# Optimization experiments

Hardware: AMD Instinct MI355X
Metric: run time of the kernel (lower is better)

The kernel has to match this reference:

```python
import jax, jax.numpy as jnp
import numpy as np

B, SENSORY, STATE, MOTOR = 4096, 64, 128, 32
ODE_UNFOLDS = 6
EPS = 1e-8
ELAPSED_TIME = 1.0


def setup_inputs() -> dict:
    key = jax.random.key(0)
    ks = jax.random.split(key, 20)
    u = lambda k, shape, lo, hi: jax.random.uniform(k, shape, jnp.float32, lo, hi)
    sign = lambda k, shape: jnp.where(jax.random.bernoulli(k, 0.5, shape), 1.0, -1.0).astype(jnp.float32)
    mask = lambda k, shape: (jax.random.uniform(k, shape) < 0.75).astype(jnp.float32)
    return {
        "inputs": jax.random.normal(ks[0], (B, SENSORY), jnp.float32),
        "states": jax.random.normal(ks[1], (B, STATE), jnp.float32),
        "gleak": u(ks[2], (STATE,), 0.001, 1.0),
        "vleak": u(ks[3], (STATE,), -0.2, 0.2),
        "cm": u(ks[4], (STATE,), 0.4, 0.6),
        "w": u(ks[5], (STATE, STATE), 0.001, 1.0),
        "sigma": u(ks[6], (STATE, STATE), 3.0, 8.0),
        "mu": u(ks[7], (STATE, STATE), 0.3, 0.8),
        "erev": sign(ks[8], (STATE, STATE)),
        "sensory_w": u(ks[9], (SENSORY, STATE), 0.001, 1.0),
        "sensory_sigma": u(ks[10], (SENSORY, STATE), 3.0, 8.0),
        "sensory_mu": u(ks[11], (SENSORY, STATE), 0.3, 0.8),
        "sensory_erev": sign(ks[12], (SENSORY, STATE)),
        "sparsity_mask": mask(ks[13], (STATE, STATE)),
        "sensory_sparsity_mask": mask(ks[14], (SENSORY, STATE)),
        "input_w": jnp.ones((SENSORY,), jnp.float32),
        "input_b": jnp.zeros((SENSORY,), jnp.float32),
        "output_w": jnp.ones((MOTOR,), jnp.float32),
        "output_b": jnp.zeros((MOTOR,), jnp.float32),
    }


def _syn_sigmoid(v_pre, mu, sigma):
    # v_pre: [B, P] -> [B, P, 1]; mu/sigma: [P, S]
    return jax.nn.sigmoid(sigma * (v_pre[..., None] - mu))


def reference(inputs, states, gleak, vleak, cm, w, sigma, mu, erev,
              sensory_w, sensory_sigma, sensory_mu, sensory_erev,
              sparsity_mask, sensory_sparsity_mask,
              input_w, input_b, output_w, output_b):
    # input mapping (affine); make_positive_fn = Identity (explicit constraints)
    x = inputs * input_w + input_b

    # sensory contributions (computed once, shared across unfolds)
    sens_act = sensory_w * _syn_sigmoid(x, sensory_mu, sensory_sigma)  # [B, In, S]
    sens_act = sens_act * sensory_sparsity_mask
    w_num_sensory = jnp.sum(sens_act * sensory_erev, axis=1)  # [B, S]
    w_den_sensory = jnp.sum(sens_act, axis=1)                 # [B, S]

    cm_t = cm / (ELAPSED_TIME / ODE_UNFOLDS)  # [S]

    v_pre = states
    for _ in range(ODE_UNFOLDS):
        w_act = w * _syn_sigmoid(v_pre, mu, sigma)   # [B, S, S]
        w_act = w_act * sparsity_mask
        w_numerator = jnp.sum(w_act * erev, axis=1) + w_num_sensory
        w_denominator = jnp.sum(w_act, axis=1) + w_den_sensory
        numerator = cm_t * v_pre + gleak * vleak + w_numerator
        denominator = cm_t + gleak + w_denominator
        v_pre = numerator / (denominator + EPS)

    # output mapping: slice motor neurons, then affine
    output = v_pre[:, :MOTOR] * output_w + output_b
    return output, v_pre
```

## Files before the change

kernel.cpp:

```cpp
#include <hip/hip_runtime.h>

#define LOG2E 1.4426950408889634f

constexpr int Bsz = 4096, Ssz = 128, Isz = 64, MOTOR = 32;
constexpr int BT = 4, NT = 256, R = 2;

__global__ void ltc_prep(const float* __restrict__ w, const float* __restrict__ sigma,
                         const float* __restrict__ mu, const float* __restrict__ erev,
                         const float* __restrict__ smask,
                         const float* __restrict__ sw, const float* __restrict__ ssig,
                         const float* __restrict__ smu, const float* __restrict__ serev,
                         const float* __restrict__ ssmask,
                         float4* __restrict__ Tm, float4* __restrict__ Ts)
{
  int idx = blockIdx.x * blockDim.x + threadIdx.x;
  if (idx < 32 * Ssz) {
    int q = idx >> 7, s = idx & 127;
    float4 a, b, wv;
    #pragma unroll
    for (int jj = 0; jj < 4; ++jj) {
      int e = (q * 4 + jj) * Ssz + s;
      float sg = sigma[e];
      (&a.x)[jj] = -sg * LOG2E;
      (&b.x)[jj] = sg * mu[e] * LOG2E;
      (&wv.x)[jj] = w[e] * smask[e] * erev[e];
    }
    Tm[(q * 3 + 0) * Ssz + s] = a;
    Tm[(q * 3 + 1) * Ssz + s] = b;
    Tm[(q * 3 + 2) * Ssz + s] = wv;
  } else if (idx < 32 * Ssz + 16 * Ssz) {
    int k = idx - 32 * Ssz;
    int q = k >> 7, s = k & 127;
    float4 a, b, wv;
    #pragma unroll
    for (int jj = 0; jj < 4; ++jj) {
      int e = (q * 4 + jj) * Ssz + s;
      float sg = ssig[e];
      (&a.x)[jj] = -sg * LOG2E;
      (&b.x)[jj] = sg * smu[e] * LOG2E;
      (&wv.x)[jj] = sw[e] * ssmask[e] * serev[e];
    }
    Ts[(q * 3 + 0) * Ssz + s] = a;
    Ts[(q * 3 + 1) * Ssz + s] = b;
    Ts[(q * 3 + 2) * Ssz + s] = wv;
  }
}

__launch_bounds__(NT, 4)
__global__ void ltc_main(const float* __restrict__ inputs, const float* __restrict__ states,
                         const float* __restrict__ gleak, const float* __restrict__ vleak,
                         const float* __restrict__ cmv,
                         const float* __restrict__ iw, const float* __restrict__ ib,
                         const float* __restrict__ ow, const float* __restrict__ ob,
                         const float4* __restrict__ Tm, const float4* __restrict__ Ts,
                         float* __restrict__ out)
{
  __shared__ float vsh[2][BT][Ssz];
  __shared__ float xsh[BT][Isz];

  const int t = threadIdx.x;
  const int s = t & 127;
  const int r0 = (t >> 7) * R;
  const int b0 = blockIdx.x * BT;

  { int r = t >> 6, i = t & 63;
    xsh[r][i] = inputs[(b0 + r) * Isz + i] * iw[i] + ib[i]; }
  for (int k = t; k < BT * Ssz; k += NT) {
    int r = k >> 7, ss = k & 127;
    vsh[0][r][ss] = states[(b0 + r) * Ssz + ss];
  }
  const float cmt = cmv[s] * 6.0f;
  const float gl = gleak[s];
  const float gv = gl * vleak[s];
  const float dbase = cmt + gl + 1e-8f;
  __syncthreads();

  float sn[R] = {0.f, 0.f}, sd[R] = {0.f, 0.f};
  {
    const float4* pb = Ts + 1 * Ssz + s;
    #pragma unroll 2
    for (int q = 0; q < 16; ++q) {
      float4 a4 = pb[-Ssz], b4 = pb[0], w4 = pb[Ssz];
      pb += 3 * Ssz;
      #pragma unroll
      for (int r = 0; r < R; ++r) {
        float4 xq = *(const float4*)&xsh[r0 + r][q * 4];
        #pragma unroll
        for (int jj = 0; jj < 4; ++jj) {
          float arg = fmaf((&a4.x)[jj], (&xq.x)[jj], (&b4.x)[jj]);
          float u = __builtin_amdgcn_exp2f(arg);
          float sig = __builtin_amdgcn_rcpf(1.0f + u);
          sn[r] = fmaf((&w4.x)[jj], sig, sn[r]);
          sd[r] = fmaf(fabsf((&w4.x)[jj]), sig, sd[r]);
        }
      }
    }
  }

  #pragma unroll 1
  for (int it = 0; it < 6; ++it) {
    const int cur = it & 1;
    const float* vcur = &vsh[cur][0][0];
    float num[R], den[R];
    #pragma unroll
    for (int r = 0; r < R; ++r) { num[r] = sn[r]; den[r] = sd[r]; }

    const float4* pb = Tm + 1 * Ssz + s;
    #pragma unroll 2
    for (int q = 0; q < 32; ++q) {
      float4 a4 = pb[-Ssz], b4 = pb[0], w4 = pb[Ssz];
      pb += 3 * Ssz;
      #pragma unroll
      for (int r = 0; r < R; ++r) {
        float4 vq = *(const float4*)&vcur[(r0 + r) * Ssz + q * 4];
        #pragma unroll
        for (int jj = 0; jj < 4; ++jj) {
          float arg = fmaf((&a4.x)[jj], (&vq.x)[jj], (&b4.x)[jj]);
          float u = __builtin_amdgcn_exp2f(arg);
          float sig = __builtin_amdgcn_rcpf(1.0f + u);
          num[r] = fmaf((&w4.x)[jj], sig, num[r]);
          den[r] = fmaf(fabsf((&w4.x)[jj]), sig, den[r]);
        }
      }
    }

    #pragma unroll
    for (int r = 0; r < R; ++r) {
      float vo = vcur[(r0 + r) * Ssz + s];
      vsh[cur ^ 1][r0 + r][s] =
          (fmaf(cmt, vo, gv) + num[r]) * __builtin_amdgcn_rcpf(dbase + den[r]);
    }
    __syncthreads();
  }

  for (int k = t; k < BT * Ssz; k += NT) {
    int r = k >> 7, ss = k & 127;
    out[Bsz * MOTOR + (b0 + r) * Ssz + ss] = vsh[0][r][ss];
  }
  if (t < BT * MOTOR) {
    int r = t >> 5, m = t & 31;
    out[(b0 + r) * MOTOR + m] = fmaf(vsh[0][r][m], ow[m], ob[m]);
  }
}

extern "C" void kernel_launch(void* const* d_in, const int* in_sizes, int n_in,
                              void* d_out, int out_size, void* d_ws, size_t ws_size,
                              hipStream_t stream) {
  const float* inputs = (const float*)d_in[0];
  const float* states = (const float*)d_in[1];
  const float* gleak  = (const float*)d_in[2];
  const float* vleak  = (const float*)d_in[3];
  const float* cmv    = (const float*)d_in[4];
  const float* w      = (const float*)d_in[5];
  const float* sigma  = (const float*)d_in[6];
  const float* mu     = (const float*)d_in[7];
  const float* erev   = (const float*)d_in[8];
  const float* sw     = (const float*)d_in[9];
  const float* ssig   = (const float*)d_in[10];
  const float* smu    = (const float*)d_in[11];
  const float* serev  = (const float*)d_in[12];
  const float* smask  = (const float*)d_in[13];
  const float* ssmask = (const float*)d_in[14];
  const float* iw     = (const float*)d_in[15];
  const float* ib     = (const float*)d_in[16];
  const float* ow     = (const float*)d_in[17];
  const float* ob     = (const float*)d_in[18];

  char* ws = (char*)d_ws;
  float4* Tm = (float4*)ws;
  float4* Ts = (float4*)(ws + 196608);
  float* out = (float*)d_out;

  constexpr int prep_items = 32 * Ssz + 16 * Ssz;
  ltc_prep<<<(prep_items + 255) / 256, 256, 0, stream>>>(
      w, sigma, mu, erev, smask, sw, ssig, smu, serev, ssmask, Tm, Ts);
  ltc_main<<<Bsz / BT, NT, 0, stream>>>(
      inputs, states, gleak, vleak, cmv, iw, ib, ow, ob, Tm, Ts, out);
}
```

Before: 113.6 us.

## Pair sigmoid reciprocals and software-prefetch next parameter tile

Computes the sigmoids in pairs, so one reciprocal of the product of two denominators serves both, replacing four transcendental rcp ops per quad with two plus a few multiplies. It also prefetches the next quad's a/b/w float4 parameters one iteration ahead in both the sensory and recurrent loops, with a peeled final iteration. This cuts pressure on the transcendental unit and hides global/L2 load latency, at the cost of more registers. Multiplying two large denominators could overflow to inf and slightly change numerics for extreme arguments.

```diff
diff --git a/kernel.cpp b/kernel.cpp
--- a/kernel.cpp
+++ b/kernel.cpp
@@ -46,6 +46,23 @@
   }
 }
 
+__device__ __forceinline__ void sig_quad(float4 a4, float4 b4, float4 w4, float4 vq,
+                                         float& num, float& den)
+{
+  float t0 = 1.0f + __builtin_amdgcn_exp2f(fmaf(a4.x, vq.x, b4.x));
+  float t1 = 1.0f + __builtin_amdgcn_exp2f(fmaf(a4.y, vq.y, b4.y));
+  float t2 = 1.0f + __builtin_amdgcn_exp2f(fmaf(a4.z, vq.z, b4.z));
+  float t3 = 1.0f + __builtin_amdgcn_exp2f(fmaf(a4.w, vq.w, b4.w));
+  float r01 = __builtin_amdgcn_rcpf(t0 * t1);
+  float r23 = __builtin_amdgcn_rcpf(t2 * t3);
+  float s0 = t1 * r01, s1 = t0 * r01;
+  float s2 = t3 * r23, s3 = t2 * r23;
+  num = fmaf(w4.x, s0, num); den = fmaf(fabsf(w4.x), s0, den);
+  num = fmaf(w4.y, s1, num); den = fmaf(fabsf(w4.y), s1, den);
+  num = fmaf(w4.z, s2, num); den = fmaf(fabsf(w4.z), s2, den);
+  num = fmaf(w4.w, s3, num); den = fmaf(fabsf(w4.w), s3, den);
+}
+
 __launch_bounds__(NT, 4)
 __global__ void ltc_main(const float* __restrict__ inputs, const float* __restrict__ states,
                          const float* __restrict__ gleak, const float* __restrict__ vleak,
@@ -78,22 +95,22 @@
   float sn[R] = {0.f, 0.f}, sd[R] = {0.f, 0.f};
   {
     const float4* pb = Ts + 1 * Ssz + s;
+    float4 a4 = pb[-Ssz], b4 = pb[0], w4 = pb[Ssz];
     #pragma unroll 2
-    for (int q = 0; q < 16; ++q) {
-      float4 a4 = pb[-Ssz], b4 = pb[0], w4 = pb[Ssz];
+    for (int q = 0; q < 15; ++q) {
+      float4 an = pb[2 * Ssz], bn = pb[3 * Ssz], wn = pb[4 * Ssz];
       pb += 3 * Ssz;
       #pragma unroll
       for (int r = 0; r < R; ++r) {
         float4 xq = *(const float4*)&xsh[r0 + r][q * 4];
-        #pragma unroll
-        for (int jj = 0; jj < 4; ++jj) {
-          float arg = fmaf((&a4.x)[jj], (&xq.x)[jj], (&b4.x)[jj]);
-          float u = __builtin_amdgcn_exp2f(arg);
-          float sig = __builtin_amdgcn_rcpf(1.0f + u);
-          sn[r] = fmaf((&w4.x)[jj], sig, sn[r]);
-          sd[r] = fmaf(fabsf((&w4.x)[jj]), sig, sd[r]);
-        }
+        sig_quad(a4, b4, w4, xq, sn[r], sd[r]);
       }
+      a4 = an; b4 = bn; w4 = wn;
+    }
+    #pragma unroll
+    for (int r = 0; r < R; ++r) {
+      float4 xq = *(const float4*)&xsh[r0 + r][15 * 4];
+      sig_quad(a4, b4, w4, xq, sn[r], sd[r]);
     }
   }
 
@@ -106,22 +123,22 @@
     for (int r = 0; r < R; ++r) { num[r] = sn[r]; den[r] = sd[r]; }
 
     const float4* pb = Tm + 1 * Ssz + s;
+    float4 a4 = pb[-Ssz], b4 = pb[0], w4 = pb[Ssz];
     #pragma unroll 2
-    for (int q = 0; q < 32; ++q) {
-      float4 a4 = pb[-Ssz], b4 = pb[0], w4 = pb[Ssz];
+    for (int q = 0; q < 31; ++q) {
+      float4 an = pb[2 * Ssz], bn = pb[3 * Ssz], wn = pb[4 * Ssz];
       pb += 3 * Ssz;
       #pragma unroll
       for (int r = 0; r < R; ++r) {
         float4 vq = *(const float4*)&vcur[(r0 + r) * Ssz + q * 4];
-        #pragma unroll
-        for (int jj = 0; jj < 4; ++jj) {
-          float arg = fmaf((&a4.x)[jj], (&vq.x)[jj], (&b4.x)[jj]);
-          float u = __builtin_amdgcn_exp2f(arg);
-          float sig = __builtin_amdgcn_rcpf(1.0f + u);
-          num[r] = fmaf((&w4.x)[jj], sig, num[r]);
-          den[r] = fmaf(fabsf((&w4.x)[jj]), sig, den[r]);
-        }
+        sig_quad(a4, b4, w4, vq, num[r], den[r]);
       }
+      a4 = an; b4 = bn; w4 = wn;
+    }
+    #pragma unroll
+    for (int r = 0; r < R; ++r) {
+      float4 vq = *(const float4*)&vcur[(r0 + r) * Ssz + 31 * 4];
+      sig_quad(a4, b4, w4, vq, num[r], den[r]);
     }
 
     #pragma unroll
```

Measured after the change: 122.1 us. 1.07x slower.

## Stage recurrent sigmoid coefficients in LDS and double batch rows per block

Applied to the files above, without the earlier changes.

The per-synapse A and B coefficient tables are split into separate planes and copied into 128 KB of dynamic shared memory once per block. The weight plane is still read from global memory, which cuts global/L2 traffic across the six ODE unfolds. The block grows to 512 threads and 8 batch rows, which halves the grid size, and loop unroll factors rise to 4. The large LDS footprint means only one block fits per CU, so occupancy drops sharply and the per-block copy adds fixed cost.

```diff
diff --git a/kernel.cpp b/kernel.cpp
--- a/kernel.cpp
+++ b/kernel.cpp
@@ -3,7 +3,8 @@
 #define LOG2E 1.4426950408889634f
 
 constexpr int Bsz = 4096, Ssz = 128, Isz = 64, MOTOR = 32;
-constexpr int BT = 4, NT = 256, R = 2;
+constexpr int BT = 8, NT = 512, R = 2;
+constexpr int SMEM_BYTES = 65536 + 65536 + 8192 + 2048;
 
 __global__ void ltc_prep(const float* __restrict__ w, const float* __restrict__ sigma,
                          const float* __restrict__ mu, const float* __restrict__ erev,
@@ -11,7 +12,10 @@
                          const float* __restrict__ sw, const float* __restrict__ ssig,
                          const float* __restrict__ smu, const float* __restrict__ serev,
                          const float* __restrict__ ssmask,
-                         float4* __restrict__ Tm, float4* __restrict__ Ts)
+                         float4* __restrict__ Apl, float4* __restrict__ Bpl,
+                         float4* __restrict__ Wpl,
+                         float4* __restrict__ Asen, float4* __restrict__ Bsen,
+                         float4* __restrict__ Wsen)
 {
   int idx = blockIdx.x * blockDim.x + threadIdx.x;
   if (idx < 32 * Ssz) {
@@ -25,9 +29,7 @@
       (&b.x)[jj] = sg * mu[e] * LOG2E;
       (&wv.x)[jj] = w[e] * smask[e] * erev[e];
     }
-    Tm[(q * 3 + 0) * Ssz + s] = a;
-    Tm[(q * 3 + 1) * Ssz + s] = b;
-    Tm[(q * 3 + 2) * Ssz + s] = wv;
+    Apl[idx] = a; Bpl[idx] = b; Wpl[idx] = wv;
   } else if (idx < 32 * Ssz + 16 * Ssz) {
     int k = idx - 32 * Ssz;
     int q = k >> 7, s = k & 127;
@@ -40,33 +42,44 @@
       (&b.x)[jj] = sg * smu[e] * LOG2E;
       (&wv.x)[jj] = sw[e] * ssmask[e] * serev[e];
     }
-    Ts[(q * 3 + 0) * Ssz + s] = a;
-    Ts[(q * 3 + 1) * Ssz + s] = b;
-    Ts[(q * 3 + 2) * Ssz + s] = wv;
+    Asen[k] = a; Bsen[k] = b; Wsen[k] = wv;
   }
 }
 
-__launch_bounds__(NT, 4)
+__launch_bounds__(NT, 2)
 __global__ void ltc_main(const float* __restrict__ inputs, const float* __restrict__ states,
                          const float* __restrict__ gleak, const float* __restrict__ vleak,
                          const float* __restrict__ cmv,
                          const float* __restrict__ iw, const float* __restrict__ ib,
                          const float* __restrict__ ow, const float* __restrict__ ob,
-                         const float4* __restrict__ Tm, const float4* __restrict__ Ts,
+                         const float4* __restrict__ Apl, const float4* __restrict__ Bpl,
+                         const float4* __restrict__ Wpl,
+                         const float4* __restrict__ Asen, const float4* __restrict__ Bsen,
+                         const float4* __restrict__ Wsen,
                          float* __restrict__ out)
 {
-  __shared__ float vsh[2][BT][Ssz];
-  __shared__ float xsh[BT][Isz];
+  extern __shared__ char smem[];
+  float4* Al = (float4*)smem;
+  float4* Bl = (float4*)(smem + 65536);
+  float (*vsh)[BT][Ssz] = (float (*)[BT][Ssz])(smem + 131072);
+  float (*xsh)[Isz] = (float (*)[Isz])(smem + 139264);
 
   const int t = threadIdx.x;
   const int s = t & 127;
   const int r0 = (t >> 7) * R;
   const int b0 = blockIdx.x * BT;
 
+  #pragma unroll
+  for (int k = 0; k < 8; ++k) {
+    Al[k * NT + t] = Apl[k * NT + t];
+    Bl[k * NT + t] = Bpl[k * NT + t];
+  }
   { int r = t >> 6, i = t & 63;
     xsh[r][i] = inputs[(b0 + r) * Isz + i] * iw[i] + ib[i]; }
-  for (int k = t; k < BT * Ssz; k += NT) {
-    int r = k >> 7, ss = k & 127;
+  #pragma unroll
+  for (int k = 0; k < 2; ++k) {
+    int kk = k * NT + t;
+    int r = kk >> 7, ss = kk & 127;
     vsh[0][r][ss] = states[(b0 + r) * Ssz + ss];
   }
   const float cmt = cmv[s] * 6.0f;
@@ -76,23 +89,21 @@
   __syncthreads();
 
   float sn[R] = {0.f, 0.f}, sd[R] = {0.f, 0.f};
-  {
-    const float4* pb = Ts + 1 * Ssz + s;
-    #pragma unroll 2
-    for (int q = 0; q < 16; ++q) {
-      float4 a4 = pb[-Ssz], b4 = pb[0], w4 = pb[Ssz];
-      pb += 3 * Ssz;
+  #pragma unroll 4
+  for (int q = 0; q < 16; ++q) {
+    float4 a4 = Asen[q * Ssz + s];
+    float4 b4 = Bsen[q * Ssz + s];
+    float4 w4 = Wsen[q * Ssz + s];
+    #pragma unroll
+    for (int r = 0; r < R; ++r) {
+      float4 xq = *(const float4*)&xsh[r0 + r][q * 4];
       #pragma unroll
-      for (int r = 0; r < R; ++r) {
-        float4 xq = *(const float4*)&xsh[r0 + r][q * 4];
-        #pragma unroll
-        for (int jj = 0; jj < 4; ++jj) {
-          float arg = fmaf((&a4.x)[jj], (&xq.x)[jj], (&b4.x)[jj]);
-          float u = __builtin_amdgcn_exp2f(arg);
-          float sig = __builtin_amdgcn_rcpf(1.0f + u);
-          sn[r] = fmaf((&w4.x)[jj], sig, sn[r]);
-          sd[r] = fmaf(fabsf((&w4.x)[jj]), sig, sd[r]);
-        }
+      for (int jj = 0; jj < 4; ++jj) {
+        float arg = fmaf((&a4.x)[jj], (&xq.x)[jj], (&b4.x)[jj]);
+        float u = __builtin_amdgcn_exp2f(arg);
+        float sig = __builtin_amdgcn_rcpf(1.0f + u);
+        sn[r] = fmaf((&w4.x)[jj], sig, sn[r]);
+        sd[r] = fmaf(fabsf((&w4.x)[jj]), sig, sd[r]);
       }
     }
   }
@@ -105,11 +116,11 @@
     #pragma unroll
     for (int r = 0; r < R; ++r) { num[r] = sn[r]; den[r] = sd[r]; }
 
-    const float4* pb = Tm + 1 * Ssz + s;
-    #pragma unroll 2
+    #pragma unroll 4
     for (int q = 0; q < 32; ++q) {
-      float4 a4 = pb[-Ssz], b4 = pb[0], w4 = pb[Ssz];
-      pb += 3 * Ssz;
+      float4 w4 = Wpl[q * Ssz + s];
+      float4 a4 = Al[q * Ssz + s];
+      float4 b4 = Bl[q * Ssz + s];
       #pragma unroll
       for (int r = 0; r < R; ++r) {
         float4 vq = *(const float4*)&vcur[(r0 + r) * Ssz + q * 4];
@@ -133,8 +144,10 @@
     __syncthreads();
   }
 
-  for (int k = t; k < BT * Ssz; k += NT) {
-    int r = k >> 7, ss = k & 127;
+  #pragma unroll
+  for (int k = 0; k < 2; ++k) {
+    int kk = k * NT + t;
+    int r = kk >> 7, ss = kk & 127;
     out[Bsz * MOTOR + (b0 + r) * Ssz + ss] = vsh[0][r][ss];
   }
   if (t < BT * MOTOR) {
@@ -167,13 +180,23 @@
   const float* ob     = (const float*)d_in[18];
 
   char* ws = (char*)d_ws;
-  float4* Tm = (float4*)ws;
-  float4* Ts = (float4*)(ws + 196608);
+  float4* Apl  = (float4*)ws;
+  float4* Bpl  = (float4*)(ws + 65536);
+  float4* Wpl  = (float4*)(ws + 131072);
+  float4* Asen = (float4*)(ws + 196608);
+  float4* Bsen = (float4*)(ws + 229376);
+  float4* Wsen = (float4*)(ws + 262144);
   float* out = (float*)d_out;
+
+  static_assert(SMEM_BYTES <= 160 * 1024, "LDS budget");
+  hipFuncSetAttribute((const void*)ltc_main,
+                      hipFuncAttributeMaxDynamicSharedMemorySize, SMEM_BYTES);
 
   constexpr int prep_items = 32 * Ssz + 16 * Ssz;
   ltc_prep<<<(prep_items + 255) / 256, 256, 0, stream>>>(
-      w, sigma, mu, erev, smask, sw, ssig, smu, serev, ssmask, Tm, Ts);
-  ltc_main<<<Bsz / BT, NT, 0, stream>>>(
-      inputs, states, gleak, vleak, cmv, iw, ib, ow, ob, Tm, Ts, out);
+      w, sigma, mu, erev, smask, sw, ssig, smu, serev, ssmask,
+      Apl, Bpl, Wpl, Asen, Bsen, Wsen);
+  ltc_main<<<Bsz / BT, NT, SMEM_BYTES, stream>>>(
+      inputs, states, gleak, vleak, cmv, iw, ib, ow, ob,
+      Apl, Bpl, Wpl, Asen, Bsen, Wsen, out);
 }
```

New measurement: 119.9 us. 5.5% more time.
